# Performance work log

Measured on AMD Instinct MI355X. Metric: run time of the kernel, lower is better.

The kernel has to match this reference:

```python
import jax, jax.numpy as jnp
import numpy as np

B, DX, DY, H = 512, 128, 128, 512


def setup_inputs() -> dict:
    key = jax.random.key(0)
    ks = jax.random.split(key, 6)
    x = jax.random.normal(ks[0], (B, DX), dtype=jnp.float32)
    y = jax.random.normal(ks[1], (B, DY), dtype=jnp.float32)
    # MLP params: Linear(DX+DY, H) -> ReLU -> Linear(H, H) -> ReLU -> Linear(H, 1)
    W1 = jax.random.normal(ks[2], (DX + DY, H), dtype=jnp.float32) / np.sqrt(DX + DY)
    b1 = jnp.zeros((H,), dtype=jnp.float32)
    W2 = jax.random.normal(ks[3], (H, H), dtype=jnp.float32) / np.sqrt(H)
    b2 = jnp.zeros((H,), dtype=jnp.float32)
    W3 = jax.random.normal(ks[4], (H, 1), dtype=jnp.float32) / np.sqrt(H)
    b3 = jnp.zeros((1,), dtype=jnp.float32)
    return {"x": x, "y": y, "W1": W1, "b1": b1, "W2": W2, "b2": b2, "W3": W3, "b3": b3}


def reference(x, y, W1, b1, W2, b2, W3, b3):
    # scores[i, j] = MLP(concat(x_i, y_j)).
    # The first linear layer is separable in x and y: split W1 and broadcast-add,
    # avoiding materializing the [B^2, DX+DY] concat tensor.
    dx = x.shape[-1]
    W1x, W1y = W1[:dx], W1[dx:]
    hx = x @ W1x                      # [B, H]
    hy = y @ W1y                      # [B, H]
    h1 = jax.nn.relu(hx[:, None, :] + hy[None, :, :] + b1)   # [B, B, H]
    h2 = jax.nn.relu(jnp.einsum('ijh,hk->ijk', h1, W2) + b2)  # [B, B, H]
    scores = jnp.einsum('ijh,ho->ijo', h2, W3) + b3           # [B, B, 1]
    return scores[..., 0]             # [B, B]
```

## Files before the change

### kernel.cpp

```cpp
#include <hip/hip_runtime.h>
#include <hip/hip_bf16.h>

typedef __bf16 bf16x8 __attribute__((ext_vector_type(8)));
typedef float  f32x4  __attribute__((ext_vector_type(4)));

#define B_  512
#define DX_ 128
#define H_  512

__global__ __launch_bounds__(256) void pack_kernel(
    const float* __restrict__ x, const float* __restrict__ y,
    const float* __restrict__ W1, const float* __restrict__ W2,
    __bf16* __restrict__ PAx, __bf16* __restrict__ PAy,
    __bf16* __restrict__ PW1x, __bf16* __restrict__ PW1y,
    __bf16* __restrict__ PW2)
{
    int gid = blockIdx.x * 256 + threadIdx.x;
    if (gid < 16384) {
        const float* src = (gid < 8192) ? x : y;
        __bf16* dst = (gid < 8192) ? PAx : PAy;
        int u = gid & 8191;
        int mt = u >> 8, ks = (u >> 6) & 3, l = u & 63;
        int row = mt * 16 + (l & 15);
        int k = ks * 32 + ((l >> 4) << 3);
        const float* p = src + row * DX_ + k;
        bf16x8 v;
        #pragma unroll
        for (int j = 0; j < 8; ++j) v[j] = (__bf16)p[j];
        *(bf16x8*)(dst + u * 8) = v;
    } else if (gid < 32768) {
        int u = gid - 16384;
        int which = u >> 13;
        u &= 8191;
        int ks = u >> 11, nt = (u >> 6) & 31, l = u & 63;
        int k = ks * 32 + ((l >> 4) << 3);
        int col = nt * 16 + (l & 15);
        const float* p = W1 + (which * 128 + k) * H_ + col;
        __bf16* dst = which ? PW1y : PW1x;
        bf16x8 v;
        #pragma unroll
        for (int j = 0; j < 8; ++j) v[j] = (__bf16)p[j * H_];
        *(bf16x8*)(dst + u * 8) = v;
    } else {
        int u = gid - 32768;
        int ks = u >> 11, nt = (u >> 6) & 31, l = u & 63;
        int k = ks * 32 + ((l >> 4) << 3);
        int col = nt * 16 + (l & 15);
        const float* p = W2 + k * H_ + col;
        bf16x8 v;
        #pragma unroll
        for (int j = 0; j < 8; ++j) v[j] = (__bf16)p[j * H_];
        *(bf16x8*)(PW2 + u * 8) = v;
    }
}

__global__ __launch_bounds__(256) void hxy_kernel(
    const __bf16* __restrict__ PAx, const __bf16* __restrict__ PAy,
    const __bf16* __restrict__ PW1x, const __bf16* __restrict__ PW1y,
    const float* __restrict__ b1,
    float* __restrict__ hx, float* __restrict__ hyb)
{
    int task = blockIdx.z;
    const __bf16* PA = task ? PAy : PAx;
    const __bf16* PW = task ? PW1y : PW1x;
    float* outp = task ? hyb : hx;
    int bm = blockIdx.y;
    int bn = blockIdx.x;
    int tid = threadIdx.x;
    int w = tid >> 6, lane = tid & 63;

    f32x4 acc[4][2] = {};
    #pragma unroll
    for (int ks = 0; ks < 4; ++ks) {
        bf16x8 af[4];
        #pragma unroll
        for (int mt = 0; mt < 4; ++mt)
            af[mt] = *(const bf16x8*)(PA + (((bm * 4 + mt) * 4 + ks) * 64 + lane) * 8);
        #pragma unroll
        for (int nt = 0; nt < 2; ++nt) {
            bf16x8 bf = *(const bf16x8*)(PW + ((ks * 32 + bn * 8 + w * 2 + nt) * 64 + lane) * 8);
            #pragma unroll
            for (int mt = 0; mt < 4; ++mt)
                acc[mt][nt] = __builtin_amdgcn_mfma_f32_16x16x32_bf16(af[mt], bf, acc[mt][nt], 0, 0, 0);
        }
    }
    #pragma unroll
    for (int nt = 0; nt < 2; ++nt) {
        int col = bn * 128 + (w * 2 + nt) * 16 + (lane & 15);
        float badd = task ? b1[col] : 0.f;
        #pragma unroll
        for (int mt = 0; mt < 4; ++mt) {
            #pragma unroll
            for (int r = 0; r < 4; ++r) {
                int row = bm * 64 + mt * 16 + ((lane >> 4) << 2) + r;
                outp[row * H_ + col] = acc[mt][nt][r] + badd;
            }
        }
    }
}

__global__ __launch_bounds__(512, 2) void critic_kernel(
    const float* __restrict__ hx, const float* __restrict__ hyb,
    const __bf16* __restrict__ PW2,
    const float* __restrict__ b2, const float* __restrict__ W3,
    const float* __restrict__ b3, float* __restrict__ out)
{
    __shared__ float hx_s[16 * 516];
    __shared__ float hy_s[8 * 516];
    __shared__ __align__(16) char h1_s[128 * 64];
    __shared__ float sc_s[128];

    int tid = threadIdx.x;
    int lane = tid & 63, wid = tid >> 6;
    int mw = wid >> 2, nw = wid & 3;
    int bj = blockIdx.x, bi = blockIdx.y;

    for (int idx = tid; idx < 16 * 128; idx += 512) {
        int r = idx >> 7, c4 = (idx & 127) << 2;
        *(float4*)&hx_s[r * 516 + c4] = *(const float4*)&hx[(bi * 16 + r) * H_ + c4];
    }
    for (int idx = tid; idx < 8 * 128; idx += 512) {
        int r = idx >> 7, c4 = (idx & 127) << 2;
        *(float4*)&hy_s[r * 516 + c4] = *(const float4*)&hyb[(bj * 8 + r) * H_ + c4];
    }

    int grow = tid >> 2, q = tid & 3;
    const float* px = &hx_s[(grow >> 3) * 516 + q * 8];
    const float* py = &hy_s[(grow & 7) * 516 + q * 8];
    char* wptr = h1_s + grow * 64 + ((q << 4) ^ ((grow & 3) << 4));

    int aoff[4];
    #pragma unroll
    for (int mt = 0; mt < 4; ++mt) {
        int arow = mw * 64 + mt * 16 + (lane & 15);
        int slot = (lane >> 4) ^ (arow & 3);
        aoff[mt] = arow * 64 + (slot << 4);
    }

    f32x4 acc[4][8] = {};

    for (int ks = 0; ks < 16; ++ks) {
        __syncthreads();
        {
            const float4 a0 = *(const float4*)(px + ks * 32);
            const float4 a1 = *(const float4*)(px + ks * 32 + 4);
            const float4 c0 = *(const float4*)(py + ks * 32);
            const float4 c1 = *(const float4*)(py + ks * 32 + 4);
            bf16x8 hv;
            hv[0] = (__bf16)fmaxf(a0.x + c0.x, 0.f);
            hv[1] = (__bf16)fmaxf(a0.y + c0.y, 0.f);
            hv[2] = (__bf16)fmaxf(a0.z + c0.z, 0.f);
            hv[3] = (__bf16)fmaxf(a0.w + c0.w, 0.f);
            hv[4] = (__bf16)fmaxf(a1.x + c1.x, 0.f);
            hv[5] = (__bf16)fmaxf(a1.y + c1.y, 0.f);
            hv[6] = (__bf16)fmaxf(a1.z + c1.z, 0.f);
            hv[7] = (__bf16)fmaxf(a1.w + c1.w, 0.f);
            *(bf16x8*)wptr = hv;
        }
        __syncthreads();
        bf16x8 af[4];
        #pragma unroll
        for (int mt = 0; mt < 4; ++mt)
            af[mt] = *(const bf16x8*)(h1_s + aoff[mt]);
        const __bf16* pb = PW2 + ((ks * 32 + nw * 8) * 64 + lane) * 8;
        #pragma unroll
        for (int nt = 0; nt < 8; ++nt) {
            bf16x8 bf = *(const bf16x8*)(pb + nt * 64 * 8);
            #pragma unroll
            for (int mt = 0; mt < 4; ++mt)
                acc[mt][nt] = __builtin_amdgcn_mfma_f32_16x16x32_bf16(af[mt], bf, acc[mt][nt], 0, 0, 0);
        }
    }

    __syncthreads();
    if (tid < 128) sc_s[tid] = 0.f;
    __syncthreads();

    float b2v[8], w3v[8];
    #pragma unroll
    for (int nt = 0; nt < 8; ++nt) {
        int col = nw * 128 + nt * 16 + (lane & 15);
        b2v[nt] = b2[col];
        w3v[nt] = W3[col];
    }
    #pragma unroll
    for (int mt = 0; mt < 4; ++mt) {
        #pragma unroll
        for (int r = 0; r < 4; ++r) {
            float s = 0.f;
            #pragma unroll
            for (int nt = 0; nt < 8; ++nt) {
                float h2 = acc[mt][nt][r] + b2v[nt];
                h2 = fmaxf(h2, 0.f);
                s += h2 * w3v[nt];
            }
            s += __shfl_xor(s, 1);
            s += __shfl_xor(s, 2);
            s += __shfl_xor(s, 4);
            s += __shfl_xor(s, 8);
            if ((lane & 15) == 0)
                atomicAdd(&sc_s[mw * 64 + mt * 16 + ((lane >> 4) << 2) + r], s);
        }
    }
    __syncthreads();
    if (tid < 128) {
        int i = bi * 16 + (tid >> 3);
        int j = bj * 8 + (tid & 7);
        out[i * B_ + j] = sc_s[tid] + b3[0];
    }
}

extern "C" void kernel_launch(void* const* d_in, const int* in_sizes, int n_in,
                              void* d_out, int out_size, void* d_ws, size_t ws_size,
                              hipStream_t stream)
{
    const float* x  = (const float*)d_in[0];
    const float* y  = (const float*)d_in[1];
    const float* W1 = (const float*)d_in[2];
    const float* b1 = (const float*)d_in[3];
    const float* W2 = (const float*)d_in[4];
    const float* b2 = (const float*)d_in[5];
    const float* W3 = (const float*)d_in[6];
    const float* b3 = (const float*)d_in[7];
    float* out = (float*)d_out;

    char* ws = (char*)d_ws;
    float*  hx   = (float*)(ws);
    float*  hyb  = (float*)(ws + 1048576);
    __bf16* PW2  = (__bf16*)(ws + 2097152);
    __bf16* PAx  = (__bf16*)(ws + 2621440);
    __bf16* PAy  = (__bf16*)(ws + 2752512);
    __bf16* PW1x = (__bf16*)(ws + 2883584);
    __bf16* PW1y = (__bf16*)(ws + 3014656);

    hipLaunchKernelGGL(pack_kernel, dim3(256), dim3(256), 0, stream,
                       x, y, W1, W2, PAx, PAy, PW1x, PW1y, PW2);
    hipLaunchKernelGGL(hxy_kernel, dim3(4, 8, 2), dim3(256), 0, stream,
                       PAx, PAy, PW1x, PW1y, b1, hx, hyb);
    hipLaunchKernelGGL(critic_kernel, dim3(64, 32), dim3(512), 0, stream,
                       hx, hyb, PW2, b2, W3, b3, out);
}
```

Baseline: 231.7 us.

## Merge prep kernels, switch to 32x32 MFMA, triple-buffer h1 with staggered waves

```diff
diff --git a/kernel.cpp b/kernel.cpp
--- a/kernel.cpp
+++ b/kernel.cpp
@@ -3,85 +3,71 @@
 
 typedef __bf16 bf16x8 __attribute__((ext_vector_type(8)));
 typedef float  f32x4  __attribute__((ext_vector_type(4)));
+typedef float  f32x16 __attribute__((ext_vector_type(16)));
 
 #define B_  512
 #define DX_ 128
 #define H_  512
 
-__global__ __launch_bounds__(256) void pack_kernel(
+__global__ __launch_bounds__(256) void prep_kernel(
     const float* __restrict__ x, const float* __restrict__ y,
     const float* __restrict__ W1, const float* __restrict__ W2,
-    __bf16* __restrict__ PAx, __bf16* __restrict__ PAy,
-    __bf16* __restrict__ PW1x, __bf16* __restrict__ PW1y,
-    __bf16* __restrict__ PW2)
+    const float* __restrict__ b1,
+    __bf16* __restrict__ PW2, float* __restrict__ hx, float* __restrict__ hyb)
 {
-    int gid = blockIdx.x * 256 + threadIdx.x;
-    if (gid < 16384) {
-        const float* src = (gid < 8192) ? x : y;
-        __bf16* dst = (gid < 8192) ? PAx : PAy;
-        int u = gid & 8191;
-        int mt = u >> 8, ks = (u >> 6) & 3, l = u & 63;
-        int row = mt * 16 + (l & 15);
-        int k = ks * 32 + ((l >> 4) << 3);
-        const float* p = src + row * DX_ + k;
-        bf16x8 v;
-        #pragma unroll
-        for (int j = 0; j < 8; ++j) v[j] = (__bf16)p[j];
-        *(bf16x8*)(dst + u * 8) = v;
-    } else if (gid < 32768) {
-        int u = gid - 16384;
-        int which = u >> 13;
-        u &= 8191;
-        int ks = u >> 11, nt = (u >> 6) & 31, l = u & 63;
-        int k = ks * 32 + ((l >> 4) << 3);
-        int col = nt * 16 + (l & 15);
-        const float* p = W1 + (which * 128 + k) * H_ + col;
-        __bf16* dst = which ? PW1y : PW1x;
-        bf16x8 v;
-        #pragma unroll
-        for (int j = 0; j < 8; ++j) v[j] = (__bf16)p[j * H_];
-        *(bf16x8*)(dst + u * 8) = v;
-    } else {
-        int u = gid - 32768;
-        int ks = u >> 11, nt = (u >> 6) & 31, l = u & 63;
-        int k = ks * 32 + ((l >> 4) << 3);
-        int col = nt * 16 + (l & 15);
+    int blk = blockIdx.x;
+    int tid = threadIdx.x;
+    if (blk < 128) {
+        int u   = blk * 256 + tid;
+        int ks2 = u >> 10;
+        int rem = u & 1023;
+        int nt  = rem >> 6;
+        int l   = rem & 63;
+        int k   = ks2 * 16 + ((l >> 5) << 3);
+        int col = nt * 32 + (l & 31);
         const float* p = W2 + k * H_ + col;
         bf16x8 v;
         #pragma unroll
         for (int j = 0; j < 8; ++j) v[j] = (__bf16)p[j * H_];
         *(bf16x8*)(PW2 + u * 8) = v;
-    }
-}
-
-__global__ __launch_bounds__(256) void hxy_kernel(
-    const __bf16* __restrict__ PAx, const __bf16* __restrict__ PAy,
-    const __bf16* __restrict__ PW1x, const __bf16* __restrict__ PW1y,
-    const float* __restrict__ b1,
-    float* __restrict__ hx, float* __restrict__ hyb)
-{
-    int task = blockIdx.z;
-    const __bf16* PA = task ? PAy : PAx;
-    const __bf16* PW = task ? PW1y : PW1x;
+        return;
+    }
+    int b    = blk - 128;
+    int task = b >> 5;
+    int rem  = b & 31;
+    int bm   = rem >> 2, bn = rem & 3;
+    const float* A  = task ? y : x;
+    const float* Wp = W1 + task * DX_ * H_;
     float* outp = task ? hyb : hx;
-    int bm = blockIdx.y;
-    int bn = blockIdx.x;
-    int tid = threadIdx.x;
     int w = tid >> 6, lane = tid & 63;
 
     f32x4 acc[4][2] = {};
     #pragma unroll
     for (int ks = 0; ks < 4; ++ks) {
+        int k0 = ks * 32 + ((lane >> 4) << 3);
         bf16x8 af[4];
         #pragma unroll
-        for (int mt = 0; mt < 4; ++mt)
-            af[mt] = *(const bf16x8*)(PA + (((bm * 4 + mt) * 4 + ks) * 64 + lane) * 8);
+        for (int mt = 0; mt < 4; ++mt) {
+            int row = bm * 64 + mt * 16 + (lane & 15);
+            const float* pa = A + row * DX_ + k0;
+            f32x4 q0 = *(const f32x4*)pa;
+            f32x4 q1 = *(const f32x4*)(pa + 4);
+            #pragma unroll
+            for (int j = 0; j < 4; ++j) {
+                af[mt][j]     = (__bf16)q0[j];
+                af[mt][j + 4] = (__bf16)q1[j];
+            }
+        }
         #pragma unroll
         for (int nt = 0; nt < 2; ++nt) {
-            bf16x8 bf = *(const bf16x8*)(PW + ((ks * 32 + bn * 8 + w * 2 + nt) * 64 + lane) * 8);
+            int col = bn * 128 + (w * 2 + nt) * 16 + (lane & 15);
+            const float* pb = Wp + k0 * H_ + col;
+            bf16x8 bv;
+            #pragma unroll
+            for (int j = 0; j < 8; ++j) bv[j] = (__bf16)pb[j * H_];
             #pragma unroll
             for (int mt = 0; mt < 4; ++mt)
-                acc[mt][nt] = __builtin_amdgcn_mfma_f32_16x16x32_bf16(af[mt], bf, acc[mt][nt], 0, 0, 0);
+                acc[mt][nt] = __builtin_amdgcn_mfma_f32_16x16x32_bf16(af[mt], bv, acc[mt][nt], 0, 0, 0);
         }
     }
     #pragma unroll
@@ -107,7 +93,7 @@
 {
     __shared__ float hx_s[16 * 516];
     __shared__ float hy_s[8 * 516];
-    __shared__ __align__(16) char h1_s[128 * 64];
+    __shared__ __align__(16) char h1_s[3 * 8192];
     __shared__ float sc_s[128];
 
     int tid = threadIdx.x;
@@ -117,89 +103,107 @@
 
     for (int idx = tid; idx < 16 * 128; idx += 512) {
         int r = idx >> 7, c4 = (idx & 127) << 2;
-        *(float4*)&hx_s[r * 516 + c4] = *(const float4*)&hx[(bi * 16 + r) * H_ + c4];
+        *(f32x4*)&hx_s[r * 516 + c4] = *(const f32x4*)&hx[(bi * 16 + r) * H_ + c4];
     }
     for (int idx = tid; idx < 8 * 128; idx += 512) {
         int r = idx >> 7, c4 = (idx & 127) << 2;
-        *(float4*)&hy_s[r * 516 + c4] = *(const float4*)&hyb[(bj * 8 + r) * H_ + c4];
-    }
+        *(f32x4*)&hy_s[r * 516 + c4] = *(const f32x4*)&hyb[(bj * 8 + r) * H_ + c4];
+    }
+    if (tid < 128) sc_s[tid] = 0.f;
 
     int grow = tid >> 2, q = tid & 3;
     const float* px = &hx_s[(grow >> 3) * 516 + q * 8];
     const float* py = &hy_s[(grow & 7) * 516 + q * 8];
-    char* wptr = h1_s + grow * 64 + ((q << 4) ^ ((grow & 3) << 4));
-
-    int aoff[4];
-    #pragma unroll
-    for (int mt = 0; mt < 4; ++mt) {
-        int arow = mw * 64 + mt * 16 + (lane & 15);
-        int slot = (lane >> 4) ^ (arow & 3);
-        aoff[mt] = arow * 64 + (slot << 4);
-    }
-
-    f32x4 acc[4][8] = {};
-
+    const int woff = grow * 64 + ((q ^ ((grow >> 1) & 3)) << 4);
+
+    int aoff[2][2];
+    #pragma unroll
+    for (int t = 0; t < 2; ++t)
+        #pragma unroll
+        for (int mt = 0; mt < 2; ++mt) {
+            int row  = mw * 64 + mt * 32 + (lane & 31);
+            int slot = (t * 2 + (lane >> 5)) ^ ((row >> 1) & 3);
+            aoff[t][mt] = row * 64 + (slot << 4);
+        }
+
+    f32x16 acc[2][4] = {};
+
+    auto GEN = [&](int g) {
+        const f32x4 a0 = *(const f32x4*)(px + g * 32);
+        const f32x4 a1 = *(const f32x4*)(px + g * 32 + 4);
+        const f32x4 c0 = *(const f32x4*)(py + g * 32);
+        const f32x4 c1 = *(const f32x4*)(py + g * 32 + 4);
+        f32x4 s0 = a0 + c0, s1 = a1 + c1;
+        bf16x8 hv;
+        #pragma unroll
+        for (int j = 0; j < 4; ++j) {
+            hv[j]     = (__bf16)fmaxf(s0[j], 0.f);
+            hv[j + 4] = (__bf16)fmaxf(s1[j], 0.f);
+        }
+        *(bf16x8*)(h1_s + (g % 3) * 8192 + woff) = hv;
+    };
+
+    auto STEP = [&](int ks) {
+        const char* base = h1_s + (ks % 3) * 8192;
+        bf16x8 a00 = *(const bf16x8*)(base + aoff[0][0]);
+        bf16x8 a01 = *(const bf16x8*)(base + aoff[0][1]);
+        bf16x8 a10 = *(const bf16x8*)(base + aoff[1][0]);
+        bf16x8 a11 = *(const bf16x8*)(base + aoff[1][1]);
+        const __bf16* pb = PW2 + ((ks * 2) * 16 + nw * 4) * 512 + lane * 8;
+        #pragma unroll
+        for (int t = 0; t < 2; ++t) {
+            #pragma unroll
+            for (int nt = 0; nt < 4; ++nt) {
+                bf16x8 bv = *(const bf16x8*)(pb + t * 8192 + nt * 512);
+                acc[0][nt] = __builtin_amdgcn_mfma_f32_32x32x16_bf16(t ? a10 : a00, bv, acc[0][nt], 0, 0, 0);
+                acc[1][nt] = __builtin_amdgcn_mfma_f32_32x32x16_bf16(t ? a11 : a01, bv, acc[1][nt], 0, 0, 0);
+            }
+        }
+    };
+
+    __syncthreads();
+    GEN(0);
+    GEN(1);
+    __syncthreads();
+
+    #pragma unroll
     for (int ks = 0; ks < 16; ++ks) {
-        __syncthreads();
-        {
-            const float4 a0 = *(const float4*)(px + ks * 32);
-            const float4 a1 = *(const float4*)(px + ks * 32 + 4);
-            const float4 c0 = *(const float4*)(py + ks * 32);
-            const float4 c1 = *(const float4*)(py + ks * 32 + 4);
-            bf16x8 hv;
-            hv[0] = (__bf16)fmaxf(a0.x + c0.x, 0.f);
-            hv[1] = (__bf16)fmaxf(a0.y + c0.y, 0.f);
-            hv[2] = (__bf16)fmaxf(a0.z + c0.z, 0.f);
-            hv[3] = (__bf16)fmaxf(a0.w + c0.w, 0.f);
-            hv[4] = (__bf16)fmaxf(a1.x + c1.x, 0.f);
-            hv[5] = (__bf16)fmaxf(a1.y + c1.y, 0.f);
-            hv[6] = (__bf16)fmaxf(a1.z + c1.z, 0.f);
-            hv[7] = (__bf16)fmaxf(a1.w + c1.w, 0.f);
-            *(bf16x8*)wptr = hv;
-        }
-        __syncthreads();
-        bf16x8 af[4];
-        #pragma unroll
-        for (int mt = 0; mt < 4; ++mt)
-            af[mt] = *(const bf16x8*)(h1_s + aoff[mt]);
-        const __bf16* pb = PW2 + ((ks * 32 + nw * 8) * 64 + lane) * 8;
-        #pragma unroll
-        for (int nt = 0; nt < 8; ++nt) {
-            bf16x8 bf = *(const bf16x8*)(pb + nt * 64 * 8);
-            #pragma unroll
-            for (int mt = 0; mt < 4; ++mt)
-                acc[mt][nt] = __builtin_amdgcn_mfma_f32_16x16x32_bf16(af[mt], bf, acc[mt][nt], 0, 0, 0);
-        }
-    }
-
-    __syncthreads();
-    if (tid < 128) sc_s[tid] = 0.f;
-    __syncthreads();
-
-    float b2v[8], w3v[8];
-    #pragma unroll
-    for (int nt = 0; nt < 8; ++nt) {
-        int col = nw * 128 + nt * 16 + (lane & 15);
+        if (mw == 0) {
+            STEP(ks);
+            if (ks < 14) GEN(ks + 2);
+        } else {
+            if (ks < 14) GEN(ks + 2);
+            STEP(ks);
+        }
+        if (ks < 15) __syncthreads();
+    }
+
+    float b2v[4], w3v[4];
+    #pragma unroll
+    for (int nt = 0; nt < 4; ++nt) {
+        int col = nw * 128 + nt * 32 + (lane & 31);
         b2v[nt] = b2[col];
         w3v[nt] = W3[col];
     }
     #pragma unroll
-    for (int mt = 0; mt < 4; ++mt) {
-        #pragma unroll
-        for (int r = 0; r < 4; ++r) {
+    for (int mt = 0; mt < 2; ++mt) {
+        #pragma unroll
+        for (int r = 0; r < 16; ++r) {
             float s = 0.f;
             #pragma unroll
-            for (int nt = 0; nt < 8; ++nt) {
-                float h2 = acc[mt][nt][r] + b2v[nt];
-                h2 = fmaxf(h2, 0.f);
+            for (int nt = 0; nt < 4; ++nt) {
+                float h2 = fmaxf(acc[mt][nt][r] + b2v[nt], 0.f);
                 s += h2 * w3v[nt];
             }
             s += __shfl_xor(s, 1);
             s += __shfl_xor(s, 2);
             s += __shfl_xor(s, 4);
             s += __shfl_xor(s, 8);
-            if ((lane & 15) == 0)
-                atomicAdd(&sc_s[mw * 64 + mt * 16 + ((lane >> 4) << 2) + r], s);
+            s += __shfl_xor(s, 16);
+            if ((lane & 31) == 0) {
+                int prow = mw * 64 + mt * 32 + ((r & 3) + 8 * (r >> 2)) + ((lane >> 5) << 2);
+                atomicAdd(&sc_s[prow], s);
+            }
         }
     }
     __syncthreads();
@@ -225,18 +229,12 @@
     float* out = (float*)d_out;
 
     char* ws = (char*)d_ws;
-    float*  hx   = (float*)(ws);
-    float*  hyb  = (float*)(ws + 1048576);
-    __bf16* PW2  = (__bf16*)(ws + 2097152);
-    __bf16* PAx  = (__bf16*)(ws + 2621440);
-    __bf16* PAy  = (__bf16*)(ws + 2752512);
-    __bf16* PW1x = (__bf16*)(ws + 2883584);
-    __bf16* PW1y = (__bf16*)(ws + 3014656);
-
-    hipLaunchKernelGGL(pack_kernel, dim3(256), dim3(256), 0, stream,
-                       x, y, W1, W2, PAx, PAy, PW1x, PW1y, PW2);
-    hipLaunchKernelGGL(hxy_kernel, dim3(4, 8, 2), dim3(256), 0, stream,
-                       PAx, PAy, PW1x, PW1y, b1, hx, hyb);
+    float*  hx  = (float*)(ws);
+    float*  hyb = (float*)(ws + 1048576);
+    __bf16* PW2 = (__bf16*)(ws + 2097152);
+
+    hipLaunchKernelGGL(prep_kernel, dim3(192), dim3(256), 0, stream,
+                       x, y, W1, W2, b1, PW2, hx, hyb);
     hipLaunchKernelGGL(critic_kernel, dim3(64, 32), dim3(512), 0, stream,
                        hx, hyb, PW2, b2, W3, b3, out);
 }
```

After: 261.4 us. 1.13x slower.
